# Kernel optimization log

Hardware: AMD Instinct MI355X
Metric: run time of the kernel (lower is better)

## Reference

```python
import jax, jax.numpy as jnp
import numpy as np

B, T, D = 2, 2048, 2048
H, DH = 16, 128
FG = 5461
EPS = 1e-5
ROPE_BASE = 10000.0


def rmsnorm(x, w):
    rms = jax.lax.rsqrt(jnp.mean(x * x, axis=-1, keepdims=True) + EPS)
    return x * rms * w


def rotate_half(x):
    x1 = x[..., ::2]
    x2 = x[..., 1::2]
    return jnp.stack((-x2, x1), axis=-1).reshape(x.shape)


def rope_tables(t_len, dh, dtype):
    inv_freq = 1.0 / (ROPE_BASE ** (np.arange(0, dh, 2, dtype=np.float32) / dh))
    t = np.arange(t_len, dtype=np.float32)
    freqs = np.outer(t, inv_freq)                 # [T, dh/2]
    emb = np.repeat(freqs, 2, axis=-1)            # repeat_interleave -> [T, dh]
    return jnp.asarray(np.cos(emb), dtype), jnp.asarray(np.sin(emb), dtype)


def setup_inputs() -> dict:
    key = jax.random.key(0)
    ks = jax.random.split(key, 8)
    s_attn = 1.0 / np.sqrt(D)
    s_gate = 1.0 / np.sqrt(D)
    s_proj = 1.0 / np.sqrt(FG)
    return {
        "x": jax.random.normal(ks[0], (B, T, D), jnp.float32),
        "norm1_w": jnp.ones((D,), jnp.float32),
        "norm2_w": jnp.ones((D,), jnp.float32),
        "c_attn_w": jax.random.normal(ks[1], (3 * D, D), jnp.float32) * s_attn,
        "c_proj_w": jax.random.normal(ks[2], (D, D), jnp.float32) * s_attn,
        "c_gate_w": jax.random.normal(ks[3], (FG, D), jnp.float32) * s_gate,
        "c_val_w": jax.random.normal(ks[4], (FG, D), jnp.float32) * s_gate,
        "c_mlp_proj_w": jax.random.normal(ks[5], (D, FG), jnp.float32) * s_proj,
    }


def block(x, norm1_w, norm2_w, c_attn_w, c_proj_w, c_gate_w, c_val_w, c_mlp_proj_w):
    # ---- attention branch (pre-norm) ----
    h = rmsnorm(x, norm1_w)
    qkv = h @ c_attn_w.T                                   # [B,T,3D]
    qkv = qkv.reshape(B, T, 3, H, DH).transpose(2, 0, 3, 1, 4)
    q, k, v = qkv[0], qkv[1], qkv[2]                       # [B,H,T,DH]
    cos, sin = rope_tables(T, DH, x.dtype)                 # [T,DH]
    q = q * cos + rotate_half(q) * sin
    k = k * cos + rotate_half(k) * sin
    att = jnp.einsum("bhqd,bhkd->bhqk", q, k) * (1.0 / np.sqrt(DH))
    causal = jnp.tril(jnp.ones((T, T), bool))
    att = jnp.where(causal, att, -jnp.inf)
    att = jax.nn.softmax(att, axis=-1)
    y = jnp.einsum("bhqk,bhkd->bhqd", att, v)              # [B,H,T,DH]
    y = y.transpose(0, 2, 1, 3).reshape(B, T, D)
    x = x + y @ c_proj_w.T
    # ---- MLP branch (pre-norm, SwiGLU) ----
    h = rmsnorm(x, norm2_w)
    gate = jax.nn.silu(h @ c_gate_w.T)                     # [B,T,FG]
    val = h @ c_val_w.T
    x = x + (gate * val) @ c_mlp_proj_w.T
    return x


def reference(x, norm1_w, norm2_w, c_attn_w, c_proj_w, c_gate_w, c_val_w, c_mlp_proj_w):
    return block(x, norm1_w, norm2_w, c_attn_w, c_proj_w, c_gate_w, c_val_w, c_mlp_proj_w)
```

## Files before the change

### kernel.cpp

```cpp
#include <hip/hip_runtime.h>
#include <hip/hip_bf16.h>
#include <stdint.h>

typedef __bf16 bf16_t;
typedef __bf16 bf16x8 __attribute__((ext_vector_type(8)));
typedef float  f32x4  __attribute__((ext_vector_type(4)));

#define DEV __device__ __forceinline__

constexpr int   Bn = 2, Tn = 2048, Dn = 2048, Hn = 16, DHn = 128;
constexpr int   BTn = Bn * Tn;
constexpr int   TD3 = 3 * Dn;
constexpr int   FGn = 5461, FGPn = 5504;
constexpr float EPSf   = 1e-5f;
constexpr float LOG2E  = 1.4426950408889634f;
constexpr float ASCALE = 0.08838834764831845f;
constexpr float LN1E4  = 9.210340371976184f;

DEV void gld16(void* lds, const void* g) {
  __builtin_amdgcn_global_load_lds(
      (__attribute__((address_space(1))) void*)(void*)g,
      (__attribute__((address_space(3))) void*)lds, 16, 0, 0);
}

DEV bf16x8 dsr128(const bf16_t* p) {
  bf16x8 r;
  asm volatile("ds_read_b128 %0, %1"
               : "=v"(r)
               : "v"((const __attribute__((address_space(3))) bf16_t*)p));
  return r;
}

__global__ __launch_bounds__(256)
void rmsnorm_k(const float* __restrict__ x, const float* __restrict__ w,
               bf16_t* __restrict__ out) {
  const int row = blockIdx.x;
  const int tid = threadIdx.x;
  const float* xr = x + (size_t)row * Dn;
  float4 a = ((const float4*)xr)[tid * 2];
  float4 b = ((const float4*)xr)[tid * 2 + 1];
  float ss = a.x*a.x + a.y*a.y + a.z*a.z + a.w*a.w
           + b.x*b.x + b.y*b.y + b.z*b.z + b.w*b.w;
#pragma unroll
  for (int off = 32; off > 0; off >>= 1) ss += __shfl_xor(ss, off, 64);
  __shared__ float red[4];
  if ((tid & 63) == 0) red[tid >> 6] = ss;
  __syncthreads();
  float tot = red[0] + red[1] + red[2] + red[3];
  float rms = rsqrtf(tot * (1.0f / Dn) + EPSf);
  float4 wa = ((const float4*)w)[tid * 2];
  float4 wb = ((const float4*)w)[tid * 2 + 1];
  bf16x8 o;
  o[0] = (bf16_t)(a.x * rms * wa.x); o[1] = (bf16_t)(a.y * rms * wa.y);
  o[2] = (bf16_t)(a.z * rms * wa.z); o[3] = (bf16_t)(a.w * rms * wa.w);
  o[4] = (bf16_t)(b.x * rms * wb.x); o[5] = (bf16_t)(b.y * rms * wb.y);
  o[6] = (bf16_t)(b.z * rms * wb.z); o[7] = (bf16_t)(b.w * rms * wb.w);
  *(bf16x8*)&out[(size_t)row * Dn + tid * 8] = o;
}

__global__ __launch_bounds__(256)
void rms_fused(const float* __restrict__ x, const bf16_t* __restrict__ P0,
               const bf16_t* __restrict__ P1, const float* __restrict__ w,
               float* __restrict__ out, bf16_t* __restrict__ h) {
  const int row = blockIdx.x;
  const int tid = threadIdx.x;
  const size_t base = (size_t)row * Dn + tid * 8;
  float4 a = ((const float4*)(x + base))[0];
  float4 b = ((const float4*)(x + base))[1];
  bf16x8 p0 = *(const bf16x8*)&P0[base];
  bf16x8 p1 = *(const bf16x8*)&P1[base];
  float v[8];
  v[0] = a.x + (float)p0[0] + (float)p1[0];
  v[1] = a.y + (float)p0[1] + (float)p1[1];
  v[2] = a.z + (float)p0[2] + (float)p1[2];
  v[3] = a.w + (float)p0[3] + (float)p1[3];
  v[4] = b.x + (float)p0[4] + (float)p1[4];
  v[5] = b.y + (float)p0[5] + (float)p1[5];
  v[6] = b.z + (float)p0[6] + (float)p1[6];
  v[7] = b.w + (float)p0[7] + (float)p1[7];
  float4 o0 = {v[0], v[1], v[2], v[3]};
  float4 o1 = {v[4], v[5], v[6], v[7]};
  ((float4*)(out + base))[0] = o0;
  ((float4*)(out + base))[1] = o1;
  float ss = 0.f;
#pragma unroll
  for (int k = 0; k < 8; ++k) ss += v[k] * v[k];
#pragma unroll
  for (int off = 32; off > 0; off >>= 1) ss += __shfl_xor(ss, off, 64);
  __shared__ float red[4];
  if ((tid & 63) == 0) red[tid >> 6] = ss;
  __syncthreads();
  float tot = red[0] + red[1] + red[2] + red[3];
  float rms = rsqrtf(tot * (1.0f / Dn) + EPSf);
  float4 wa = ((const float4*)w)[tid * 2];
  float4 wb = ((const float4*)w)[tid * 2 + 1];
  bf16x8 o;
  o[0] = (bf16_t)(v[0] * rms * wa.x); o[1] = (bf16_t)(v[1] * rms * wa.y);
  o[2] = (bf16_t)(v[2] * rms * wa.z); o[3] = (bf16_t)(v[3] * rms * wa.w);
  o[4] = (bf16_t)(v[4] * rms * wb.x); o[5] = (bf16_t)(v[5] * rms * wb.y);
  o[6] = (bf16_t)(v[6] * rms * wb.z); o[7] = (bf16_t)(v[7] * rms * wb.w);
  *(bf16x8*)&h[base] = o;
}

__global__ __launch_bounds__(256)
void cvt_pad_k(const float* __restrict__ src, bf16_t* __restrict__ dst,
               int srcR, int srcC, int dstC, int n8) {
  int i = blockIdx.x * 256 + threadIdx.x;
  if (i >= n8) return;
  long base = (long)i * 8;
  int r = (int)(base / dstC);
  int c = (int)(base % dstC);
  bf16x8 o;
#pragma unroll
  for (int k = 0; k < 8; ++k) {
    int cc = c + k;
    float v = (r < srcR && cc < srcC) ? src[(size_t)r * srcC + cc] : 0.0f;
    o[k] = (bf16_t)v;
  }
  *(bf16x8*)&dst[base] = o;
}

__global__ __launch_bounds__(256)
void reduce_k(float* __restrict__ out, const bf16_t* __restrict__ P0,
              const bf16_t* __restrict__ P1) {
  int i = blockIdx.x * 256 + threadIdx.x;
  bf16x8 p0 = *(const bf16x8*)&P0[(size_t)i * 8];
  bf16x8 p1 = *(const bf16x8*)&P1[(size_t)i * 8];
  float4 o0 = ((const float4*)out)[i * 2];
  float4 o1 = ((const float4*)out)[i * 2 + 1];
  o0.x += (float)p0[0] + (float)p1[0];
  o0.y += (float)p0[1] + (float)p1[1];
  o0.z += (float)p0[2] + (float)p1[2];
  o0.w += (float)p0[3] + (float)p1[3];
  o1.x += (float)p0[4] + (float)p1[4];
  o1.y += (float)p0[5] + (float)p1[5];
  o1.z += (float)p0[6] + (float)p1[6];
  o1.w += (float)p0[7] + (float)p1[7];
  ((float4*)out)[i * 2]     = o0;
  ((float4*)out)[i * 2 + 1] = o1;
}

__global__ __launch_bounds__(512, 2)
void gemm_sk(const bf16_t* __restrict__ A, const bf16_t* __restrict__ W,
             bf16_t* __restrict__ P0, bf16_t* __restrict__ P1,
             int ldk, int klen, int ldc, int nby) {
  __shared__ __align__(128) bf16_t As[2][256 * 64];
  __shared__ __align__(128) bf16_t Bs[2][256 * 64];
  const int tid = threadIdx.x;
  const int lane = tid & 63, w = tid >> 6;
  const int wm = w >> 2, wn = w & 3;
  const int g = lane >> 4, q = lane & 15;

  const int nwg = gridDim.x;
  const int cpx = nwg >> 3;
  const int nid = (blockIdx.x & 7) * cpx + (blockIdx.x >> 3);
  const int half = nwg >> 1;
  const int s   = nid / half;
  const int rem = nid % half;
  const int bx = rem / nby, by = rem % nby;
  const int row0 = by * 256, col0 = bx * 256;
  const int kofs = s * klen;
  bf16_t* P = s ? P1 : P0;

  f32x4 acc[8][4] = {};

  const bf16_t* Asrc[4];
  const bf16_t* Wsrc[4];
  int aoff[4];
#pragma unroll
  for (int i = 0; i < 4; ++i) {
    int ci = i * 512 + tid;
    int r  = ci >> 3;
    int cs = (ci & 7) ^ (r & 7);
    Asrc[i] = A + (size_t)(row0 + r) * ldk + kofs + cs * 8;
    Wsrc[i] = W + (size_t)(col0 + r) * ldk + kofs + cs * 8;
    aoff[i] = i * 8192 + w * 1024;
  }

  int offA[2][8], offB[2][4];
#pragma unroll
  for (int kk = 0; kk < 2; ++kk) {
#pragma unroll
    for (int m = 0; m < 8; ++m) {
      int r = wm * 128 + m * 16 + q;
      offA[kk][m] = r * 128 + (((kk * 4 + g) ^ (r & 7)) * 16);
    }
#pragma unroll
    for (int n = 0; n < 4; ++n) {
      int r = wn * 64 + n * 16 + q;
      offB[kk][n] = r * 128 + (((kk * 4 + g) ^ (r & 7)) * 16);
    }
  }

  const int NT = klen >> 6;
  auto stage = [&](int T, int h) {
    const int slot = T & 1;
    const size_t kk = (size_t)T * 64;
#pragma unroll
    for (int i = 0; i < 2; ++i) {
      int rd = h * 2 + i;
      gld16((char*)As[slot] + aoff[rd], Asrc[rd] + kk);
      gld16((char*)Bs[slot] + aoff[rd], Wsrc[rd] + kk);
    }
  };

  bf16x8 af[8], bfr[4];

  auto half_rd = [&](const char* as_, const char* bs_, int kk) {
#pragma unroll
    for (int m = 0; m < 8; ++m) af[m] = dsr128((const bf16_t*)(as_ + offA[kk][m]));
#pragma unroll
    for (int n = 0; n < 4; ++n) bfr[n] = dsr128((const bf16_t*)(bs_ + offB[kk][n]));
  };
  auto mfmas = [&]() {
    asm volatile("s_waitcnt lgkmcnt(0)" ::: "memory");
    __builtin_amdgcn_sched_barrier(0);
    __builtin_amdgcn_s_setprio(1);
#pragma unroll
    for (int m = 0; m < 8; ++m)
#pragma unroll
      for (int n = 0; n < 4; ++n)
        acc[m][n] = __builtin_amdgcn_mfma_f32_16x16x32_bf16(af[m], bfr[n], acc[m][n], 0, 0, 0);
    __builtin_amdgcn_s_setprio(0);
    __builtin_amdgcn_sched_barrier(0);
  };

  stage(0, 0); stage(0, 1);
  asm volatile("s_waitcnt vmcnt(0)" ::: "memory");
  asm volatile("s_barrier" ::: "memory");

  for (int T = 0; T < NT; ++T) {
    const char* as_ = (const char*)As[T & 1];
    const char* bs_ = (const char*)Bs[T & 1];
    const bool st = (T + 1 < NT);
    half_rd(as_, bs_, 0);
    if (st) stage(T + 1, 0);
    mfmas();
    half_rd(as_, bs_, 1);
    if (st) stage(T + 1, 1);
    mfmas();
    if (st) asm volatile("s_waitcnt vmcnt(0)" ::: "memory");
    asm volatile("s_barrier" ::: "memory");
  }

#pragma unroll
  for (int m = 0; m < 8; ++m)
#pragma unroll
    for (int n = 0; n < 4; ++n)
#pragma unroll
      for (int j = 0; j < 4; ++j) {
        int r = row0 + wm * 128 + m * 16 + g * 4 + j;
        int c = col0 + wn * 64 + n * 16 + q;
        P[(size_t)r * ldc + c] = (bf16_t)acc[m][n][j];
      }
}

__global__ __launch_bounds__(512, 2)
void gemmgv(const bf16_t* __restrict__ A, const bf16_t* __restrict__ Wg,
            const bf16_t* __restrict__ Wv, bf16_t* __restrict__ Out,
            int K, int ldc, int nby) {
  __shared__ __align__(128) bf16_t As[2][256 * 64];
  __shared__ __align__(128) bf16_t Gs[2][128 * 64];
  __shared__ __align__(128) bf16_t Vs[2][128 * 64];
  const int tid = threadIdx.x;
  const int lane = tid & 63, w = tid >> 6;
  const int wm = w >> 2, wn = w & 3;
  const int g = lane >> 4, q = lane & 15;

  const int nwg = gridDim.x;
  const int cpx = nwg >> 3;
  const int nid = (blockIdx.x & 7) * cpx + (blockIdx.x >> 3);
  const int bx = nid / nby, by = nid % nby;
  const int row0 = by * 256, col0 = bx * 128;

  f32x4 accg[8][2] = {}, accv[8][2] = {};

  const bf16_t* Asrc[4];
  int aoff[4];
#pragma unroll
  for (int i = 0; i < 4; ++i) {
    int ci = i * 512 + tid;
    int r  = ci >> 3;
    int cs = (ci & 7) ^ (r & 7);
    Asrc[i] = A + (size_t)(row0 + r) * K + cs * 8;
    aoff[i] = i * 8192 + w * 1024;
  }
  const bf16_t* Gsrc[2];
  const bf16_t* Vsrc[2];
  int boff[2];
#pragma unroll
  for (int i = 0; i < 2; ++i) {
    int ci = i * 512 + tid;
    int r  = ci >> 3;
    int cs = (ci & 7) ^ (r & 7);
    Gsrc[i] = Wg + (size_t)(col0 + r) * K + cs * 8;
    Vsrc[i] = Wv + (size_t)(col0 + r) * K + cs * 8;
    boff[i] = i * 8192 + w * 1024;
  }

  int offA[2][8], offB[2][2];
#pragma unroll
  for (int kk = 0; kk < 2; ++kk) {
#pragma unroll
    for (int m = 0; m < 8; ++m) {
      int r = wm * 128 + m * 16 + q;
      offA[kk][m] = r * 128 + (((kk * 4 + g) ^ (r & 7)) * 16);
    }
#pragma unroll
    for (int n = 0; n < 2; ++n) {
      int r = wn * 32 + n * 16 + q;
      offB[kk][n] = r * 128 + (((kk * 4 + g) ^ (r & 7)) * 16);
    }
  }

  const int NT = K >> 6;
  auto stage = [&](int T, int h) {
    const int slot = T & 1;
    const size_t kk = (size_t)T * 64;
#pragma unroll
    for (int i = 0; i < 2; ++i) {
      int rd = h * 2 + i;
      gld16((char*)As[slot] + aoff[rd], Asrc[rd] + kk);
    }
    gld16((char*)Gs[slot] + boff[h], Gsrc[h] + kk);
    gld16((char*)Vs[slot] + boff[h], Vsrc[h] + kk);
  };

  bf16x8 af[8], bg[2], bv[2];

  auto half_rd = [&](const char* as_, const char* gs_, const char* vs_, int kk) {
#pragma unroll
    for (int m = 0; m < 8; ++m) af[m] = dsr128((const bf16_t*)(as_ + offA[kk][m]));
#pragma unroll
    for (int n = 0; n < 2; ++n) {
      bg[n] = dsr128((const bf16_t*)(gs_ + offB[kk][n]));
      bv[n] = dsr128((const bf16_t*)(vs_ + offB[kk][n]));
    }
  };
  auto mfmas = [&]() {
    asm volatile("s_waitcnt lgkmcnt(0)" ::: "memory");
    __builtin_amdgcn_sched_barrier(0);
    __builtin_amdgcn_s_setprio(1);
#pragma unroll
    for (int m = 0; m < 8; ++m)
#pragma unroll
      for (int n = 0; n < 2; ++n) {
        accg[m][n] = __builtin_amdgcn_mfma_f32_16x16x32_bf16(af[m], bg[n], accg[m][n], 0, 0, 0);
        accv[m][n] = __builtin_amdgcn_mfma_f32_16x16x32_bf16(af[m], bv[n], accv[m][n], 0, 0, 0);
      }
    __builtin_amdgcn_s_setprio(0);
    __builtin_amdgcn_sched_barrier(0);
  };

  stage(0, 0); stage(0, 1);
  asm volatile("s_waitcnt vmcnt(0)" ::: "memory");
  asm volatile("s_barrier" ::: "memory");

  for (int T = 0; T < NT; ++T) {
    const char* as_ = (const char*)As[T & 1];
    const char* gs_ = (const char*)Gs[T & 1];
    const char* vs_ = (const char*)Vs[T & 1];
    const bool st = (T + 1 < NT);
    half_rd(as_, gs_, vs_, 0);
    if (st) stage(T + 1, 0);
    mfmas();
    half_rd(as_, gs_, vs_, 1);
    if (st) stage(T + 1, 1);
    mfmas();
    if (st) asm volatile("s_waitcnt vmcnt(0)" ::: "memory");
    asm volatile("s_barrier" ::: "memory");
  }

#pragma unroll
  for (int m = 0; m < 8; ++m) {
#pragma unroll
    for (int n = 0; n < 2; ++n) {
#pragma unroll
      for (int j = 0; j < 4; ++j) {
        int r = row0 + wm * 128 + m * 16 + g * 4 + j;
        int c = col0 + wn * 32 + n * 16 + q;
        float gt = accg[m][n][j];
        float sg = gt / (1.0f + __expf(-gt));
        Out[(size_t)r * ldc + c] = (bf16_t)(sg * accv[m][n][j]);
      }
    }
  }
}

__global__ __launch_bounds__(256)
void rope_fused(const bf16_t* __restrict__ P0, const bf16_t* __restrict__ P1,
                bf16_t* __restrict__ Qb, bf16_t* __restrict__ Kb,
                bf16_t* __restrict__ Vt) {
  const int t0 = blockIdx.x * 32;
  const int bh = blockIdx.y;
  const int b = bh >> 4, hh = bh & 15;
  __shared__ bf16_t Vl[32][132];

#pragma unroll
  for (int it = 0; it < 2; ++it) {
    int task = threadIdx.x + it * 256;
    int tt = task >> 4, ck = task & 15, d0 = ck * 8;
    int tg = t0 + tt;
    const size_t rb = (size_t)(b * Tn + tg) * TD3 + hh * DHn + d0;
    bf16x8 q0 = *(const bf16x8*)&P0[rb];
    bf16x8 q1 = *(const bf16x8*)&P1[rb];
    bf16x8 k0 = *(const bf16x8*)&P0[rb + Dn];
    bf16x8 k1 = *(const bf16x8*)&P1[rb + Dn];
    bf16x8 v0 = *(const bf16x8*)&P0[rb + 2 * Dn];
    bf16x8 v1 = *(const bf16x8*)&P1[rb + 2 * Dn];
    bf16x8 qo, ko, vo;
#pragma unroll
    for (int p = 0; p < 4; ++p) {
      int jj = (d0 >> 1) + p;
      float fr = __expf(-((float)(2 * jj) / 128.0f) * LN1E4);
      float ang = (float)tg * fr;
      float cs = cosf(ang), sn = sinf(ang);
      float qe = (float)q0[2 * p] + (float)q1[2 * p];
      float qod = (float)q0[2 * p + 1] + (float)q1[2 * p + 1];
      float ke = (float)k0[2 * p] + (float)k1[2 * p];
      float kod = (float)k0[2 * p + 1] + (float)k1[2 * p + 1];
      qo[2 * p]     = (bf16_t)((qe * cs - qod * sn) * ASCALE);
      qo[2 * p + 1] = (bf16_t)((qod * cs + qe * sn) * ASCALE);
      ko[2 * p]     = (bf16_t)(ke * cs - kod * sn);
      ko[2 * p + 1] = (bf16_t)(kod * cs + ke * sn);
      vo[2 * p]     = (bf16_t)((float)v0[2 * p] + (float)v1[2 * p]);
      vo[2 * p + 1] = (bf16_t)((float)v0[2 * p + 1] + (float)v1[2 * p + 1]);
    }
    *(bf16x8*)&Qb[((size_t)bh * Tn + tg) * DHn + d0] = qo;
    *(bf16x8*)&Kb[((size_t)bh * Tn + tg) * DHn + d0] = ko;
    *(bf16x8*)&Vl[tt][d0] = vo;
  }
  __syncthreads();
#pragma unroll
  for (int it = 0; it < 2; ++it) {
    int task = threadIdx.x + it * 256;
    int dd = task >> 2, tc = (task & 3) * 8;
    bf16x8 ov;
#pragma unroll
    for (int i = 0; i < 8; ++i) ov[i] = Vl[tc + i][dd];
    *(bf16x8*)&Vt[((size_t)bh * DHn + dd) * Tn + t0 + tc] = ov;
  }
}

__global__ __launch_bounds__(256, 2)
void attn_k(const bf16_t* __restrict__ Qb, const bf16_t* __restrict__ Kb,
            const bf16_t* __restrict__ Vt, bf16_t* __restrict__ Y) {
  const int orig = blockIdx.x + 16 * blockIdx.y;
  const int nid  = (orig & 7) * 64 + (orig >> 3);
  const int pi = nid & 15;
  const int bh = nid >> 4;
  const int b = bh >> 4, hh = bh & 15;
  const int tid = threadIdx.x, lane = tid & 63, w = tid >> 6;
  const int g = lane >> 4, q = lane & 15;
  const int iA = pi, iB = 31 - pi;
  const int kmax = iB;

  __shared__ bf16_t Ks[2][64 * 128];
  __shared__ bf16_t Vs[2][128 * 64];
  __shared__ bf16_t Ps[4][16 * 72];

  bf16x8 aqA[4], aqB[4];
  {
    const bf16_t* QrA = Qb + ((size_t)bh * Tn + iA * 64 + w * 16 + q) * DHn;
    const bf16_t* QrB = Qb + ((size_t)bh * Tn + iB * 64 + w * 16 + q) * DHn;
#pragma unroll
    for (int s = 0; s < 4; ++s) {
      aqA[s] = *(const bf16x8*)(QrA + s * 32 + g * 8);
      aqB[s] = *(const bf16x8*)(QrB + s * 32 + g * 8);
    }
  }

  f32x4 oA[8] = {}, oB[8] = {};
  float mA[4], lA[4], mB[4], lB[4];
#pragma unroll
  for (int j = 0; j < 4; ++j) {
    mA[j] = -__builtin_inff(); lA[j] = 0.0f;
    mB[j] = -__builtin_inff(); lB[j] = 0.0f;
  }

  auto stage = [&](int buf, int kt) {
    const int k0 = kt * 64;
#pragma unroll
    for (int l = 0; l < 4; ++l) {
      int ci = (w * 4 + l) * 64 + lane;
      int kr = ci >> 4, kc = (ci & 15) ^ (kr & 7);
      gld16((char*)Ks[buf] + (w * 4 + l) * 1024,
            Kb + ((size_t)bh * Tn + k0 + kr) * DHn + kc * 8);
      int vr = ci >> 3, vc = (ci & 7) ^ (vr & 7);
      gld16((char*)Vs[buf] + (w * 4 + l) * 1024,
            Vt + ((size_t)bh * DHn + vr) * Tn + k0 + vc * 8);
    }
  };

  stage(0, 0);

  for (int kt = 0; kt <= kmax; ++kt) {
    __syncthreads();
    if (kt < kmax) stage((kt + 1) & 1, kt + 1);
    const bf16_t* ks = Ks[kt & 1];
    const bf16_t* vs = Vs[kt & 1];
    const bool actA = (kt <= iA);
    const int k0 = kt * 64;

    f32x4 saA[4] = {}, saB[4] = {};
    __builtin_amdgcn_s_setprio(1);
    if (actA) {
#pragma unroll
      for (int s = 0; s < 4; ++s) {
#pragma unroll
        for (int n = 0; n < 4; ++n) {
          bf16x8 bk = *(const bf16x8*)&ks[(n * 16 + q) * 128 + (((s * 4 + g) ^ (q & 7)) * 8)];
          saA[n] = __builtin_amdgcn_mfma_f32_16x16x32_bf16(aqA[s], bk, saA[n], 0, 0, 0);
          saB[n] = __builtin_amdgcn_mfma_f32_16x16x32_bf16(aqB[s], bk, saB[n], 0, 0, 0);
        }
      }
    } else {
#pragma unroll
      for (int s = 0; s < 4; ++s) {
#pragma unroll
        for (int n = 0; n < 4; ++n) {
          bf16x8 bk = *(const bf16x8*)&ks[(n * 16 + q) * 128 + (((s * 4 + g) ^ (q & 7)) * 8)];
          saB[n] = __builtin_amdgcn_mfma_f32_16x16x32_bf16(aqB[s], bk, saB[n], 0, 0, 0);
        }
      }
    }
    __builtin_amdgcn_s_setprio(0);

    bf16x8 paA[2], paB[2];
    auto softmax_p = [&](f32x4* sa, float* mst, float* lst, int itile,
                         bf16x8* pa, int qrow) {
      if (kt == itile) {
#pragma unroll
        for (int n = 0; n < 4; ++n)
#pragma unroll
          for (int j = 0; j < 4; ++j) {
            int kc = k0 + n * 16 + q;
            int qr = qrow + g * 4 + j;
            if (kc > qr) sa[n][j] = -1e30f;
          }
      }
      float mx[4];
#pragma unroll
      for (int j = 0; j < 4; ++j) {
        mx[j] = fmaxf(fmaxf(sa[0][j], sa[1][j]), fmaxf(sa[2][j], sa[3][j]));
#pragma unroll
        for (int off = 1; off < 16; off <<= 1)
          mx[j] = fmaxf(mx[j], __shfl_xor(mx[j], off, 16));
      }
      float ps[4][4], rsum[4];
#pragma unroll
      for (int j = 0; j < 4; ++j) rsum[j] = 0.0f;
      float mnew[4], corr[4];
#pragma unroll
      for (int j = 0; j < 4; ++j) {
        mnew[j] = fmaxf(mst[j], mx[j]);
        corr[j] = exp2f((mst[j] - mnew[j]) * LOG2E);
      }
#pragma unroll
      for (int n = 0; n < 4; ++n)
#pragma unroll
        for (int j = 0; j < 4; ++j) {
          ps[n][j] = exp2f((sa[n][j] - mnew[j]) * LOG2E);
          rsum[j] += ps[n][j];
        }
#pragma unroll
      for (int j = 0; j < 4; ++j) {
#pragma unroll
        for (int off = 1; off < 16; off <<= 1)
          rsum[j] += __shfl_xor(rsum[j], off, 16);
        lst[j] = lst[j] * corr[j] + rsum[j];
        mst[j] = mnew[j];
      }
#pragma unroll
      for (int n = 0; n < 4; ++n)
#pragma unroll
        for (int j = 0; j < 4; ++j)
          Ps[w][(g * 4 + j) * 72 + n * 16 + q] = (bf16_t)ps[n][j];
#pragma unroll
      for (int s2 = 0; s2 < 2; ++s2)
        pa[s2] = *(const bf16x8*)&Ps[w][q * 72 + s2 * 32 + g * 8];
      return corr;
    };

    float cA[4], cB[4];
    if (actA) {
      auto c = softmax_p(saA, mA, lA, iA, paA, iA * 64 + w * 16);
#pragma unroll
      for (int j = 0; j < 4; ++j) cA[j] = c[j];
#pragma unroll
      for (int n8 = 0; n8 < 8; ++n8)
#pragma unroll
        for (int j = 0; j < 4; ++j) oA[n8][j] *= cA[j];
    }
    {
      auto c = softmax_p(saB, mB, lB, iB, paB, iB * 64 + w * 16);
#pragma unroll
      for (int j = 0; j < 4; ++j) cB[j] = c[j];
#pragma unroll
      for (int n8 = 0; n8 < 8; ++n8)
#pragma unroll
        for (int j = 0; j < 4; ++j) oB[n8][j] *= cB[j];
    }

    __builtin_amdgcn_s_setprio(1);
    if (actA) {
#pragma unroll
      for (int s2 = 0; s2 < 2; ++s2)
#pragma unroll
        for (int n8 = 0; n8 < 8; ++n8) {
          bf16x8 bv = *(const bf16x8*)&vs[(n8 * 16 + q) * 64 + (((s2 * 4 + g) ^ (q & 7)) * 8)];
          oA[n8] = __builtin_amdgcn_mfma_f32_16x16x32_bf16(paA[s2], bv, oA[n8], 0, 0, 0);
          oB[n8] = __builtin_amdgcn_mfma_f32_16x16x32_bf16(paB[s2], bv, oB[n8], 0, 0, 0);
        }
    } else {
#pragma unroll
      for (int s2 = 0; s2 < 2; ++s2)
#pragma unroll
        for (int n8 = 0; n8 < 8; ++n8) {
          bf16x8 bv = *(const bf16x8*)&vs[(n8 * 16 + q) * 64 + (((s2 * 4 + g) ^ (q & 7)) * 8)];
          oB[n8] = __builtin_amdgcn_mfma_f32_16x16x32_bf16(paB[s2], bv, oB[n8], 0, 0, 0);
        }
    }
    __builtin_amdgcn_s_setprio(0);
  }

#pragma unroll
  for (int n8 = 0; n8 < 8; ++n8)
#pragma unroll
    for (int j = 0; j < 4; ++j) {
      int trA = iA * 64 + w * 16 + g * 4 + j;
      int trB = iB * 64 + w * 16 + g * 4 + j;
      Y[(size_t)(b * Tn + trA) * Dn + hh * DHn + n8 * 16 + q] =
          (bf16_t)(oA[n8][j] / lA[j]);
      Y[(size_t)(b * Tn + trB) * Dn + hh * DHn + n8 * 16 + q] =
          (bf16_t)(oB[n8][j] / lB[j]);
    }
}

extern "C" void kernel_launch(void* const* d_in, const int* in_sizes, int n_in,
                              void* d_out, int out_size, void* d_ws, size_t ws_size,
                              hipStream_t stream) {
  const float* x      = (const float*)d_in[0];
  const float* n1w    = (const float*)d_in[1];
  const float* n2w    = (const float*)d_in[2];
  const float* attn_w = (const float*)d_in[3];
  const float* proj_w = (const float*)d_in[4];
  const float* gate_w = (const float*)d_in[5];
  const float* val_w  = (const float*)d_in[6];
  const float* mlp_w  = (const float*)d_in[7];

  char* ws = (char*)d_ws;
  bf16_t* h    = (bf16_t*)(ws);
  bf16_t* bufA = (bf16_t*)(ws + 16777216);
  bf16_t* bufB = (bf16_t*)(ws + 67108864);
  bf16_t* wb   = (bf16_t*)(ws + 117440512);

  bf16_t* Pq0  = bufB;
  bf16_t* Pq1  = bufA;
  bf16_t* Qb   = wb;
  bf16_t* Kb   = (bf16_t*)d_out;
  bf16_t* Vt   = (bf16_t*)d_out + (size_t)32 * Tn * DHn;
  bf16_t* y    = h;
  bf16_t* Pp0  = bufA;
  bf16_t* Pp1  = bufA + (size_t)BTn * Dn;
  bf16_t* wbV  = bufA;
  bf16_t* gv   = bufB;
  bf16_t* Pm0  = h;
  bf16_t* Pm1  = bufA;
  float*  out  = (float*)d_out;

  rmsnorm_k<<<BTn, 256, 0, stream>>>(x, n1w, h);
  cvt_pad_k<<<(TD3 * Dn / 8 + 255) / 256, 256, 0, stream>>>(attn_w, wb, TD3, Dn, Dn, TD3 * Dn / 8);
  gemm_sk<<<768, 512, 0, stream>>>(h, wb, Pq0, Pq1, Dn, Dn / 2, TD3, BTn / 256);
  rope_fused<<<dim3(Tn / 32, 32), 256, 0, stream>>>(Pq0, Pq1, Qb, Kb, Vt);
  attn_k<<<dim3(16, 32), 256, 0, stream>>>(Qb, Kb, Vt, y);
  cvt_pad_k<<<(Dn * Dn / 8 + 255) / 256, 256, 0, stream>>>(proj_w, wb, Dn, Dn, Dn, Dn * Dn / 8);
  gemm_sk<<<256, 512, 0, stream>>>(y, wb, Pp0, Pp1, Dn, Dn / 2, Dn, BTn / 256);
  rms_fused<<<BTn, 256, 0, stream>>>(x, Pp0, Pp1, n2w, out, h);
  cvt_pad_k<<<(FGPn * Dn / 8 + 255) / 256, 256, 0, stream>>>(gate_w, wb, FGn, Dn, Dn, FGPn * Dn / 8);
  cvt_pad_k<<<(FGPn * Dn / 8 + 255) / 256, 256, 0, stream>>>(val_w, wbV, FGn, Dn, Dn, FGPn * Dn / 8);
  gemmgv<<<(FGPn / 128) * (BTn / 256), 512, 0, stream>>>(h, wb, wbV, gv, Dn, FGPn, BTn / 256);
  cvt_pad_k<<<(Dn * FGPn / 8 + 255) / 256, 256, 0, stream>>>(mlp_w, wb, Dn, FGn, FGPn, Dn * FGPn / 8);
  gemm_sk<<<256, 512, 0, stream>>>(gv, wb, Pm0, Pm1, FGPn, FGPn / 2, Dn, BTn / 256);
  reduce_k<<<BTn * Dn / 8 / 256, 256, 0, stream>>>(out, Pm0, Pm1);
}
```

Baseline: 710.2 us.

## Fuse fp32-to-bf16 weight conversion into gate/value GEMM B-tile loading

Drops the two cvt_pad_k launches that converted the gate and value weights to padded bf16. The gemmgv kernel now reads fp32 weights directly into registers, converts them to bf16 and writes them into LDS, zero-filling rows past FG. This removes a full write and re-read of the converted weights, at the cost of doubled global read bytes for the B tiles inside the GEMM, extra VGPR pressure, and register-staged loads instead of direct global-to-LDS loads, which may hurt the pipeline.

```diff
diff --git a/kernel.cpp b/kernel.cpp
--- a/kernel.cpp
+++ b/kernel.cpp
@@ -256,8 +256,8 @@
 }
 
 __global__ __launch_bounds__(512, 2)
-void gemmgv(const bf16_t* __restrict__ A, const bf16_t* __restrict__ Wg,
-            const bf16_t* __restrict__ Wv, bf16_t* __restrict__ Out,
+void gemmgv(const bf16_t* __restrict__ A, const float* __restrict__ Wg,
+            const float* __restrict__ Wv, bf16_t* __restrict__ Out,
             int K, int ldc, int nby) {
   __shared__ __align__(128) bf16_t As[2][256 * 64];
   __shared__ __align__(128) bf16_t Gs[2][128 * 64];
@@ -285,17 +285,21 @@
     Asrc[i] = A + (size_t)(row0 + r) * K + cs * 8;
     aoff[i] = i * 8192 + w * 1024;
   }
-  const bf16_t* Gsrc[2];
-  const bf16_t* Vsrc[2];
+  const float* Gsrc[2];
+  const float* Vsrc[2];
+  bool bvalid[2];
   int boff[2];
 #pragma unroll
   for (int i = 0; i < 2; ++i) {
     int ci = i * 512 + tid;
     int r  = ci >> 3;
     int cs = (ci & 7) ^ (r & 7);
-    Gsrc[i] = Wg + (size_t)(col0 + r) * K + cs * 8;
-    Vsrc[i] = Wv + (size_t)(col0 + r) * K + cs * 8;
-    boff[i] = i * 8192 + w * 1024;
+    int rg = col0 + r;
+    bvalid[i] = (rg < FGn);
+    const size_t rb = (size_t)(bvalid[i] ? rg : 0) * K + cs * 8;
+    Gsrc[i] = Wg + rb;
+    Vsrc[i] = Wv + rb;
+    boff[i] = i * 8192 + tid * 16;
   }
 
   int offA[2][8], offB[2][2];
@@ -314,7 +318,7 @@
   }
 
   const int NT = K >> 6;
-  auto stage = [&](int T, int h) {
+  auto stageA = [&](int T, int h) {
     const int slot = T & 1;
     const size_t kk = (size_t)T * 64;
 #pragma unroll
@@ -322,8 +326,39 @@
       int rd = h * 2 + i;
       gld16((char*)As[slot] + aoff[rd], Asrc[rd] + kk);
     }
-    gld16((char*)Gs[slot] + boff[h], Gsrc[h] + kk);
-    gld16((char*)Vs[slot] + boff[h], Vsrc[h] + kk);
+  };
+
+  f32x4 fG[2][2], fV[2][2];
+  auto ldB32 = [&](int T) {
+    const size_t kk = (size_t)T * 64;
+#pragma unroll
+    for (int i = 0; i < 2; ++i) {
+      if (bvalid[i]) {
+        fG[i][0] = ((const f32x4*)(Gsrc[i] + kk))[0];
+        fG[i][1] = ((const f32x4*)(Gsrc[i] + kk))[1];
+        fV[i][0] = ((const f32x4*)(Vsrc[i] + kk))[0];
+        fV[i][1] = ((const f32x4*)(Vsrc[i] + kk))[1];
+      } else {
+        fG[i][0] = f32x4{0,0,0,0}; fG[i][1] = f32x4{0,0,0,0};
+        fV[i][0] = f32x4{0,0,0,0}; fV[i][1] = f32x4{0,0,0,0};
+      }
+    }
+  };
+  auto writeB = [&](int T) {
+    const int slot = T & 1;
+#pragma unroll
+    for (int i = 0; i < 2; ++i) {
+      bf16x8 og, ov;
+#pragma unroll
+      for (int k = 0; k < 4; ++k) {
+        og[k]     = (bf16_t)fG[i][0][k];
+        og[4 + k] = (bf16_t)fG[i][1][k];
+        ov[k]     = (bf16_t)fV[i][0][k];
+        ov[4 + k] = (bf16_t)fV[i][1][k];
+      }
+      *(bf16x8*)((char*)Gs[slot] + boff[i]) = og;
+      *(bf16x8*)((char*)Vs[slot] + boff[i]) = ov;
+    }
   };
 
   bf16x8 af[8], bg[2], bv[2];
@@ -352,7 +387,10 @@
     __builtin_amdgcn_sched_barrier(0);
   };
 
-  stage(0, 0); stage(0, 1);
+  ldB32(0);
+  stageA(0, 0); stageA(0, 1);
+  writeB(0);
+  asm volatile("s_waitcnt lgkmcnt(0)" ::: "memory");
   asm volatile("s_waitcnt vmcnt(0)" ::: "memory");
   asm volatile("s_barrier" ::: "memory");
 
@@ -361,13 +399,18 @@
     const char* gs_ = (const char*)Gs[T & 1];
     const char* vs_ = (const char*)Vs[T & 1];
     const bool st = (T + 1 < NT);
+    if (st) ldB32(T + 1);
     half_rd(as_, gs_, vs_, 0);
-    if (st) stage(T + 1, 0);
+    if (st) stageA(T + 1, 0);
     mfmas();
     half_rd(as_, gs_, vs_, 1);
-    if (st) stage(T + 1, 1);
+    if (st) stageA(T + 1, 1);
     mfmas();
-    if (st) asm volatile("s_waitcnt vmcnt(0)" ::: "memory");
+    if (st) {
+      writeB(T + 1);
+      asm volatile("s_waitcnt lgkmcnt(0)" ::: "memory");
+      asm volatile("s_waitcnt vmcnt(0)" ::: "memory");
+    }
     asm volatile("s_barrier" ::: "memory");
   }
 
@@ -663,7 +706,6 @@
   bf16_t* y    = h;
   bf16_t* Pp0  = bufA;
   bf16_t* Pp1  = bufA + (size_t)BTn * Dn;
-  bf16_t* wbV  = bufA;
   bf16_t* gv   = bufB;
   bf16_t* Pm0  = h;
   bf16_t* Pm1  = bufA;
@@ -677,9 +719,7 @@
   cvt_pad_k<<<(Dn * Dn / 8 + 255) / 256, 256, 0, stream>>>(proj_w, wb, Dn, Dn, Dn, Dn * Dn / 8);
   gemm_sk<<<256, 512, 0, stream>>>(y, wb, Pp0, Pp1, Dn, Dn / 2, Dn, BTn / 256);
   rms_fused<<<BTn, 256, 0, stream>>>(x, Pp0, Pp1, n2w, out, h);
-  cvt_pad_k<<<(FGPn * Dn / 8 + 255) / 256, 256, 0, stream>>>(gate_w, wb, FGn, Dn, Dn, FGPn * Dn / 8);
-  cvt_pad_k<<<(FGPn * Dn / 8 + 255) / 256, 256, 0, stream>>>(val_w, wbV, FGn, Dn, Dn, FGPn * Dn / 8);
-  gemmgv<<<(FGPn / 128) * (BTn / 256), 512, 0, stream>>>(h, wb, wbV, gv, Dn, FGPn, BTn / 256);
+  gemmgv<<<(FGPn / 128) * (BTn / 256), 512, 0, stream>>>(h, gate_w, val_w, gv, Dn, FGPn, BTn / 256);
   cvt_pad_k<<<(Dn * FGPn / 8 + 255) / 256, 256, 0, stream>>>(mlp_w, wb, Dn, FGn, FGPn, Dn * FGPn / 8);
   gemm_sk<<<256, 512, 0, stream>>>(gv, wb, Pm0, Pm1, FGPn, FGPn / 2, Dn, BTn / 256);
   reduce_k<<<BTn * Dn / 8 / 256, 256, 0, stream>>>(out, Pm0, Pm1);
```

New measurement: 717.8 us. No clear change (+1.1%).
